# Performance work log

Hardware: AMD Instinct MI355X
Metric: run time of the kernel (lower is better)

The kernel has to match this reference:

```python
import jax, jax.numpy as jnp
import numpy as np

# dims
C = 16      # input_channels
H = 64      # hidden_channels
HID = 128   # CDEFunc hidden width (hardcoded in source)
OUT = 1     # output_channels
L = 128     # number of time knots -> L-1 spline segments
B = 2048    # batch


def setup_inputs() -> dict:
    key = jax.random.key(0)
    ks = jax.random.split(key, 9)
    n = lambda k, shape, s: (jax.random.normal(k, shape, dtype=jnp.float32) * s)
    return {
        # cubic Hermite spline coeffs: concat(a, b, two_c, three_d) along last dim
        "coeffs": n(ks[0], (B, L - 1, 4 * C), 0.1),
        "W_init": n(ks[1], (H, C), 0.2),
        "b_init": jnp.zeros((H,), jnp.float32),
        "W1": n(ks[2], (HID, H), 0.1),
        "b1": jnp.zeros((HID,), jnp.float32),
        "W2": n(ks[3], (H * C, HID), 0.05),
        "b2": jnp.zeros((H * C,), jnp.float32),
        "W_out": n(ks[4], (OUT, H), 0.1),
        "b_out": jnp.zeros((OUT,), jnp.float32),
    }


def _spline_deriv(coeffs, t):
    """dX/dt of cubic spline at scalar time t. coeffs: (B, L-1, 4C)."""
    idx = jnp.clip(jnp.floor(t).astype(jnp.int32), 0, L - 2)
    seg = jax.lax.dynamic_slice_in_dim(coeffs, idx, 1, axis=1)[:, 0]  # (B, 4C)
    a, b, two_c, three_d = jnp.split(seg, 4, axis=-1)
    fr = t - idx.astype(t.dtype) if hasattr(t, 'dtype') else t - idx
    return b + two_c * fr + three_d * (fr * fr)  # (B, C)


def reference(coeffs, W_init, b_init, W1, b1, W2, b2, W_out, b_out):
    # X(0) = a of first segment (frac = 0)
    X0 = coeffs[:, 0, :C]
    z0 = X0 @ W_init.T + b_init  # (B, H)

    def f(z, dX):
        # CDEFunc: linear-relu-linear-tanh -> (B, H, C), then contract with dX/dt
        h = jax.nn.relu(z @ W1.T + b1)
        g = jnp.tanh(h @ W2.T + b2).reshape(-1, H, C)
        return jnp.einsum('bhc,bc->bh', g, dX)

    dt = jnp.float32(1.0)  # one RK4 step per knot interval

    def step(z, t):
        d0 = _spline_deriv(coeffs, t)
        dm = _spline_deriv(coeffs, t + 0.5 * dt)
        d1 = _spline_deriv(coeffs, t + dt)
        k1 = f(z, d0)
        k2 = f(z + 0.5 * dt * k1, dm)
        k3 = f(z + 0.5 * dt * k2, dm)
        k4 = f(z + dt * k3, d1)
        return z + (dt / 6.0) * (k1 + 2.0 * k2 + 2.0 * k3 + k4), None

    ts = jnp.arange(L - 1, dtype=jnp.float32)
    zT, _ = jax.lax.scan(step, z0, ts)
    return zT @ W_out.T + b_out  # (B, OUT)
```

## Files before the change

### kernel.cpp

```cpp
#include <hip/hip_runtime.h>

#define L_DIM 128
#define BB 8

typedef _Float16 f16;
typedef _Float16 f16x4 __attribute__((ext_vector_type(4)));
typedef _Float16 f16x8 __attribute__((ext_vector_type(8)));
typedef float f32x4 __attribute__((ext_vector_type(4)));

__device__ __forceinline__ float fast_tanh_b(float x, float bk) {
    float e = __builtin_amdgcn_exp2f(fmaf(x, 2.8853900817779268f, bk));
    float r = __builtin_amdgcn_rcpf(e + 1.0f);
    return fmaf(-2.0f, r, 1.0f);
}

__attribute__((amdgpu_flat_work_group_size(512, 512), amdgpu_waves_per_eu(2)))
__global__ void
cde_kernel(const float* __restrict__ coeffs,
           const float* __restrict__ W_init, const float* __restrict__ b_init,
           const float* __restrict__ W1, const float* __restrict__ b1,
           const float* __restrict__ W2, const float* __restrict__ b2,
           const float* __restrict__ W_out, const float* __restrict__ b_out,
           float* __restrict__ out)
{
    __shared__ __align__(16) f16   z16[16][72];
    __shared__ __align__(16) f16   h16[16][136];
    __shared__ __align__(16) float zf[BB][64];
    __shared__ __align__(16) float dxb[128][16][8];
    __shared__ __align__(16) float dxm[127][16][8];

    const int tid  = threadIdx.x;
    const int blk  = blockIdx.x;
    const int lane = tid & 63;
    const int w    = tid >> 6;
    const int q    = lane >> 4;
    const int lr   = lane & 15;
    const int hh   = w * 8 + (lr & 7);
    const int chp  = lr >> 3;
    const int row0 = (q & 1) * 4 + (q >> 1) * 2;

    f16x8 w2f[8][4];
    float b2k[8];
#pragma unroll
    for (int t8 = 0; t8 < 8; ++t8) {
        const int outc = hh * 16 + 2 * t8 + chp;
        b2k[t8] = 2.8853900817779268f * b2[outc];
#pragma unroll
        for (int kc = 0; kc < 4; ++kc) {
            const float* src = W2 + (size_t)outc * 128 + kc * 32 + q * 8;
            f16x8 v;
#pragma unroll
            for (int i = 0; i < 8; ++i) v[i] = (f16)src[i];
            w2f[t8][kc] = v;
        }
    }
    f16x8 w1f[2];
#pragma unroll
    for (int kc = 0; kc < 2; ++kc) {
        const float* src = W1 + (size_t)(w * 16 + lr) * 64 + kc * 32 + q * 8;
        f16x8 v;
#pragma unroll
        for (int i = 0; i < 8; ++i) v[i] = (f16)src[i];
        w1f[kc] = v;
    }
    const float4 b1q = *(const float4*)&b1[w * 16 + q * 4];
    const f32x4 zero4 = {0.f, 0.f, 0.f, 0.f};

    float z32r[2], ksumr[2];
#pragma unroll
    for (int j = 0; j < 2; ++j) {
        const float* x0 = coeffs + (size_t)(blk * BB + row0 + j) * (L_DIM - 1) * 64;
        float a = b_init[hh];
#pragma unroll
        for (int c = 0; c < 16; ++c) a = fmaf(x0[c], W_init[hh * 16 + c], a);
        z32r[j] = a;
        ksumr[j] = 0.f;
        if (lr < 8) z16[row0 + j][hh] = (f16)a;
    }
    for (int i = tid; i < 8 * 72; i += 512) z16[8 + i / 72][i % 72] = (f16)0.f;

#pragma unroll 2
    for (int i = tid; i < 127 * 128; i += 512) {
        const int t = i >> 7, j = i & 127;
        const int c = j & 15, b = (j >> 4) & 7;
        const float* seg = coeffs + ((size_t)(blk * BB + b) * (L_DIM - 1) + t) * 64;
        const float bv = seg[16 + c], cv = seg[32 + c], dv = seg[48 + c];
        dxb[t][c][b] = bv;
        dxm[t][c][b] = fmaf(0.25f, dv, fmaf(0.5f, cv, bv));
        if (t == 126) dxb[127][c][b] = bv + cv + dv;
    }
    __syncthreads();

#define G2T(dst, T) \
    f32x4 dst = __builtin_amdgcn_mfma_f32_16x16x32_f16(af0, w2f[T][0], zero4, 0, 0, 0); \
    dst = __builtin_amdgcn_mfma_f32_16x16x32_f16(af1, w2f[T][1], dst, 0, 0, 0);         \
    dst = __builtin_amdgcn_mfma_f32_16x16x32_f16(af2, w2f[T][2], dst, 0, 0, 0);         \
    dst = __builtin_amdgcn_mfma_f32_16x16x32_f16(af3, w2f[T][3], dst, 0, 0, 0);
#define G2TAIL(src, T) {                                                  \
    float u0 = __shfl_xor(src[2], 32);                                    \
    float u1 = __shfl_xor(src[3], 32);                                    \
    float g0 = fast_tanh_b((lane < 32) ? src[0] : u0, b2k[T]);            \
    float g1 = fast_tanh_b((lane < 32) ? src[1] : u1, b2k[T]);            \
    ka0 = fmaf(g0, dvv[(T) & 3].x, ka0);                                  \
    ka1 = fmaf(g1, dvv[(T) & 3].y, ka1); }

    for (int t = 0; t < L_DIM - 1; ++t) {
#pragma unroll
        for (int s = 0; s < 4; ++s) {
            {
                f16x8 za0 = *(const f16x8*)&z16[lr][q * 8];
                f16x8 za1 = *(const f16x8*)&z16[lr][32 + q * 8];
                f32x4 hacc = __builtin_amdgcn_mfma_f32_16x16x32_f16(w1f[0], za0, zero4, 0, 0, 0);
                hacc = __builtin_amdgcn_mfma_f32_16x16x32_f16(w1f[1], za1, hacc, 0, 0, 0);
                f16x4 pp;
                pp[0] = (f16)fmaxf(hacc[0] + b1q.x, 0.f);
                pp[1] = (f16)fmaxf(hacc[1] + b1q.y, 0.f);
                pp[2] = (f16)fmaxf(hacc[2] + b1q.z, 0.f);
                pp[3] = (f16)fmaxf(hacc[3] + b1q.w, 0.f);
                *(f16x4*)&h16[lr][w * 16 + q * 4] = pp;
            }
            __syncthreads();

            const float* dxp = (s == 0) ? &dxb[t][0][0]
                             : (s == 3) ? &dxb[t + 1][0][0]
                                        : &dxm[t][0][0];
            float ka0 = 0.f, ka1 = 0.f;
#pragma unroll
            for (int hf = 0; hf < 2; ++hf) {
                float2 dvv[4];
#pragma unroll
                for (int tt = 0; tt < 4; ++tt)
                    dvv[tt] = *(const float2*)&dxp[(2 * (hf * 4 + tt) + chp) * 8 + row0];
                const f16x8 af0 = *(const f16x8*)&h16[lr][q * 8];
                const f16x8 af1 = *(const f16x8*)&h16[lr][32 + q * 8];
                const f16x8 af2 = *(const f16x8*)&h16[lr][64 + q * 8];
                const f16x8 af3 = *(const f16x8*)&h16[lr][96 + q * 8];
                G2T(a0, hf * 4 + 0)
                G2T(a1, hf * 4 + 1)
                G2TAIL(a0, hf * 4 + 0)
                G2T(a2, hf * 4 + 2)
                G2TAIL(a1, hf * 4 + 1)
                G2T(a3, hf * 4 + 3)
                G2TAIL(a2, hf * 4 + 2)
                G2TAIL(a3, hf * 4 + 3)
            }
            ka0 += __shfl_xor(ka0, 8);
            ka1 += __shfl_xor(ka1, 8);
            float zs0, zs1;
            if (s == 3) {
                z32r[0] = fmaf(ksumr[0] + ka0, 1.f / 6.f, z32r[0]); zs0 = z32r[0];
                z32r[1] = fmaf(ksumr[1] + ka1, 1.f / 6.f, z32r[1]); zs1 = z32r[1];
            } else {
                ksumr[0] = (s == 0) ? ka0 : fmaf(2.f, ka0, ksumr[0]);
                ksumr[1] = (s == 0) ? ka1 : fmaf(2.f, ka1, ksumr[1]);
                const float alpha = (s == 2) ? 1.f : 0.5f;
                zs0 = fmaf(alpha, ka0, z32r[0]);
                zs1 = fmaf(alpha, ka1, z32r[1]);
            }
            if (lr < 8) {
                z16[row0 + 0][hh] = (f16)zs0;
                z16[row0 + 1][hh] = (f16)zs1;
            }
            __syncthreads();
        }
    }

    if (lr < 8) {
        zf[row0 + 0][hh] = z32r[0];
        zf[row0 + 1][hh] = z32r[1];
    }
    __syncthreads();
    if (tid < 64) {
        const int b = lane >> 3, j0 = lane & 7;
        float p = 0.f;
#pragma unroll
        for (int m = 0; m < 8; ++m) p += zf[b][j0 + 8 * m] * W_out[j0 + 8 * m];
        p += __shfl_xor(p, 1, 64);
        p += __shfl_xor(p, 2, 64);
        p += __shfl_xor(p, 4, 64);
        if (j0 == 0) out[blk * BB + b] = p + b_out[0];
    }
}

extern "C" void kernel_launch(void* const* d_in, const int* in_sizes, int n_in,
                              void* d_out, int out_size, void* d_ws, size_t ws_size,
                              hipStream_t stream) {
    const float* coeffs = (const float*)d_in[0];
    const float* W_init = (const float*)d_in[1];
    const float* b_init = (const float*)d_in[2];
    const float* W1     = (const float*)d_in[3];
    const float* b1     = (const float*)d_in[4];
    const float* W2     = (const float*)d_in[5];
    const float* b2     = (const float*)d_in[6];
    const float* W_out  = (const float*)d_in[7];
    const float* b_out  = (const float*)d_in[8];
    cde_kernel<<<256, 512, 0, stream>>>(coeffs, W_init, b_init, W1, b1, W2, b2,
                                        W_out, b_out, (float*)d_out);
}
```

Before: 666.5 us.

## Replace block barriers with LDS flag spin-waits and split waves into two groups

Replaces both per-stage __syncthreads with LDS atomic counters and spin-waits. The 8 waves are split into two groups of four, and each group computes the full hidden layer into its own double-buffered h buffer, so the two groups only need to synchronise through the z-update counter. z16 is also double-buffered so the next stage can start without a full barrier. In exchange, each wave does twice the first-layer MFMA work, and the spin loops spend issue slots and LDS bandwidth polling. The scheme also depends on correct LDS memory ordering between waves.

```diff
diff --git a/kernel.cpp b/kernel.cpp
--- a/kernel.cpp
+++ b/kernel.cpp
@@ -12,6 +12,11 @@
     float e = __builtin_amdgcn_exp2f(fmaf(x, 2.8853900817779268f, bk));
     float r = __builtin_amdgcn_rcpf(e + 1.0f);
     return fmaf(-2.0f, r, 1.0f);
+}
+
+__device__ __forceinline__ void spin_ge(volatile int* f, int tgt) {
+    while (*f < tgt) {}
+    asm volatile("" ::: "memory");
 }
 
 __attribute__((amdgpu_flat_work_group_size(512, 512), amdgpu_waves_per_eu(2)))
@@ -23,11 +28,12 @@
            const float* __restrict__ W_out, const float* __restrict__ b_out,
            float* __restrict__ out)
 {
-    __shared__ __align__(16) f16   z16[16][72];
-    __shared__ __align__(16) f16   h16[16][136];
+    __shared__ __align__(16) f16   z16[2][16][72];
+    __shared__ __align__(16) f16   h16g[2][2][16][136];
     __shared__ __align__(16) float zf[BB][64];
     __shared__ __align__(16) float dxb[128][16][8];
     __shared__ __align__(16) float dxm[127][16][8];
+    __shared__ int sflags[4];
 
     const int tid  = threadIdx.x;
     const int blk  = blockIdx.x;
@@ -35,6 +41,8 @@
     const int w    = tid >> 6;
     const int q    = lane >> 4;
     const int lr   = lane & 15;
+    const int g    = w >> 2;
+    const int v    = w & 3;
     const int hh   = w * 8 + (lr & 7);
     const int chp  = lr >> 3;
     const int row0 = (q & 1) * 4 + (q >> 1) * 2;
@@ -48,22 +56,25 @@
 #pragma unroll
         for (int kc = 0; kc < 4; ++kc) {
             const float* src = W2 + (size_t)outc * 128 + kc * 32 + q * 8;
-            f16x8 v;
-#pragma unroll
-            for (int i = 0; i < 8; ++i) v[i] = (f16)src[i];
-            w2f[t8][kc] = v;
+            f16x8 vv;
+#pragma unroll
+            for (int i = 0; i < 8; ++i) vv[i] = (f16)src[i];
+            w2f[t8][kc] = vv;
         }
     }
-    f16x8 w1f[2];
-#pragma unroll
-    for (int kc = 0; kc < 2; ++kc) {
-        const float* src = W1 + (size_t)(w * 16 + lr) * 64 + kc * 32 + q * 8;
-        f16x8 v;
-#pragma unroll
-        for (int i = 0; i < 8; ++i) v[i] = (f16)src[i];
-        w1f[kc] = v;
-    }
-    const float4 b1q = *(const float4*)&b1[w * 16 + q * 4];
+    f16x8 w1f[2][2];
+#pragma unroll
+    for (int n = 0; n < 2; ++n)
+#pragma unroll
+        for (int kc = 0; kc < 2; ++kc) {
+            const float* src = W1 + (size_t)(v * 32 + n * 16 + lr) * 64 + kc * 32 + q * 8;
+            f16x8 vv;
+#pragma unroll
+            for (int i = 0; i < 8; ++i) vv[i] = (f16)src[i];
+            w1f[n][kc] = vv;
+        }
+    const float4 b1q0 = *(const float4*)&b1[v * 32 + q * 4];
+    const float4 b1q1 = *(const float4*)&b1[v * 32 + 16 + q * 4];
     const f32x4 zero4 = {0.f, 0.f, 0.f, 0.f};
 
     float z32r[2], ksumr[2];
@@ -75,9 +86,11 @@
         for (int c = 0; c < 16; ++c) a = fmaf(x0[c], W_init[hh * 16 + c], a);
         z32r[j] = a;
         ksumr[j] = 0.f;
-        if (lr < 8) z16[row0 + j][hh] = (f16)a;
-    }
-    for (int i = tid; i < 8 * 72; i += 512) z16[8 + i / 72][i % 72] = (f16)0.f;
+        if (lr < 8) z16[0][row0 + j][hh] = (f16)a;
+    }
+    for (int i = tid; i < 2 * 8 * 72; i += 512)
+        z16[i / (8 * 72)][8 + (i % (8 * 72)) / 72][i % 72] = (f16)0.f;
+    if (tid == 0) { sflags[0] = 0; sflags[1] = 0; sflags[2] = 0; }
 
 #pragma unroll 2
     for (int i = tid; i < 127 * 128; i += 512) {
@@ -90,6 +103,8 @@
         if (t == 126) dxb[127][c][b] = bv + cv + dv;
     }
     __syncthreads();
+
+    if (g == 1) spin_ge(&sflags[1], 4);
 
 #define G2T(dst, T) \
     f32x4 dst = __builtin_amdgcn_mfma_f32_16x16x32_f16(af0, w2f[T][0], zero4, 0, 0, 0); \
@@ -107,23 +122,37 @@
     for (int t = 0; t < L_DIM - 1; ++t) {
 #pragma unroll
         for (int s = 0; s < 4; ++s) {
+            const int e  = 4 * t + s;
+            const int eb = e & 1;
+            spin_ge(&sflags[0], 8 * e);
+
             {
-                f16x8 za0 = *(const f16x8*)&z16[lr][q * 8];
-                f16x8 za1 = *(const f16x8*)&z16[lr][32 + q * 8];
-                f32x4 hacc = __builtin_amdgcn_mfma_f32_16x16x32_f16(w1f[0], za0, zero4, 0, 0, 0);
-                hacc = __builtin_amdgcn_mfma_f32_16x16x32_f16(w1f[1], za1, hacc, 0, 0, 0);
-                f16x4 pp;
-                pp[0] = (f16)fmaxf(hacc[0] + b1q.x, 0.f);
-                pp[1] = (f16)fmaxf(hacc[1] + b1q.y, 0.f);
-                pp[2] = (f16)fmaxf(hacc[2] + b1q.z, 0.f);
-                pp[3] = (f16)fmaxf(hacc[3] + b1q.w, 0.f);
-                *(f16x4*)&h16[lr][w * 16 + q * 4] = pp;
-            }
-            __syncthreads();
+                const f16x8 zb0 = *(const f16x8*)&z16[eb][lr][q * 8];
+                const f16x8 zb1 = *(const f16x8*)&z16[eb][lr][32 + q * 8];
+#pragma unroll
+                for (int n = 0; n < 2; ++n) {
+                    f32x4 hacc = __builtin_amdgcn_mfma_f32_16x16x32_f16(w1f[n][0], zb0, zero4, 0, 0, 0);
+                    hacc = __builtin_amdgcn_mfma_f32_16x16x32_f16(w1f[n][1], zb1, hacc, 0, 0, 0);
+                    const float4 bq = n ? b1q1 : b1q0;
+                    f16x4 pp;
+                    pp[0] = (f16)fmaxf(hacc[0] + bq.x, 0.f);
+                    pp[1] = (f16)fmaxf(hacc[1] + bq.y, 0.f);
+                    pp[2] = (f16)fmaxf(hacc[2] + bq.z, 0.f);
+                    pp[3] = (f16)fmaxf(hacc[3] + bq.w, 0.f);
+                    *(f16x4*)&h16g[g][eb][lr][(2 * v + n) * 16 + q * 4] = pp;
+                }
+            }
+            asm volatile("s_waitcnt lgkmcnt(0)" ::: "memory");
+            if (lane == 0) atomicAdd((int*)&sflags[1 + g], 1);
+            spin_ge(&sflags[1 + g], 4 * (e + 1));
 
             const float* dxp = (s == 0) ? &dxb[t][0][0]
                              : (s == 3) ? &dxb[t + 1][0][0]
                                         : &dxm[t][0][0];
+            const f16x8 af0 = *(const f16x8*)&h16g[g][eb][lr][q * 8];
+            const f16x8 af1 = *(const f16x8*)&h16g[g][eb][lr][32 + q * 8];
+            const f16x8 af2 = *(const f16x8*)&h16g[g][eb][lr][64 + q * 8];
+            const f16x8 af3 = *(const f16x8*)&h16g[g][eb][lr][96 + q * 8];
             float ka0 = 0.f, ka1 = 0.f;
 #pragma unroll
             for (int hf = 0; hf < 2; ++hf) {
@@ -131,10 +160,6 @@
 #pragma unroll
                 for (int tt = 0; tt < 4; ++tt)
                     dvv[tt] = *(const float2*)&dxp[(2 * (hf * 4 + tt) + chp) * 8 + row0];
-                const f16x8 af0 = *(const f16x8*)&h16[lr][q * 8];
-                const f16x8 af1 = *(const f16x8*)&h16[lr][32 + q * 8];
-                const f16x8 af2 = *(const f16x8*)&h16[lr][64 + q * 8];
-                const f16x8 af3 = *(const f16x8*)&h16[lr][96 + q * 8];
                 G2T(a0, hf * 4 + 0)
                 G2T(a1, hf * 4 + 1)
                 G2TAIL(a0, hf * 4 + 0)
@@ -158,13 +183,15 @@
                 zs1 = fmaf(alpha, ka1, z32r[1]);
             }
             if (lr < 8) {
-                z16[row0 + 0][hh] = (f16)zs0;
-                z16[row0 + 1][hh] = (f16)zs1;
-            }
-            __syncthreads();
+                z16[eb ^ 1][row0 + 0][hh] = (f16)zs0;
+                z16[eb ^ 1][row0 + 1][hh] = (f16)zs1;
+            }
+            asm volatile("s_waitcnt lgkmcnt(0)" ::: "memory");
+            if (lane == 0) atomicAdd((int*)&sflags[0], 1);
         }
     }
 
+    __syncthreads();
     if (lr < 8) {
         zf[row0 + 0][hh] = z32r[0];
         zf[row0 + 1][hh] = z32r[1];
```

Measured after the change: 776.0 us. 1.16x slower.
